# Performance work log

Hardware: AMD Instinct MI355X
Metric: run time of the kernel (lower is better)

## Reference

```python
import jax, jax.numpy as jnp
import numpy as np

N_NODES = 100000
N_EDGES = 1600000
IN_F = 128
OUT_F = 64
DROP_P = 0.1


def setup_inputs() -> dict:
    key = jax.random.key(0)
    ks = jax.random.split(key, 7)
    x = jax.random.normal(ks[0], (N_NODES, IN_F), dtype=jnp.float32)
    row_idx = jax.random.randint(ks[1], (N_EDGES,), 0, N_NODES)
    col_idx = jax.random.randint(ks[2], (N_EDGES,), 0, N_NODES)
    # normalized-adjacency-like edge weights
    adj_vals = jax.random.uniform(ks[3], (N_EDGES,), dtype=jnp.float32)
    # deterministic dropout mask (True = keep), p = DROP_P
    drop_mask = jax.random.uniform(ks[4], (N_NODES, OUT_F)) >= DROP_P
    # nn.Linear params (PyTorch default-ish init scale)
    bound = 1.0 / np.sqrt(IN_F)
    weight = jax.random.uniform(ks[5], (IN_F, OUT_F), minval=-bound, maxval=bound, dtype=jnp.float32)
    bias = jax.random.uniform(ks[6], (OUT_F,), minval=-bound, maxval=bound, dtype=jnp.float32)
    return {"x": x, "row_idx": row_idx, "col_idx": col_idx, "adj_vals": adj_vals,
            "drop_mask": drop_mask, "weight": weight, "bias": bias}


def reference(x, row_idx, col_idx, adj_vals, drop_mask, weight, bias):
    # hidden = Linear(x)
    hidden = x @ weight + bias                      # [N, OUT_F]
    # F.dropout (training): mask + rescale by 1/(1-p)
    hidden = jnp.where(drop_mask, hidden * (1.0 / (1.0 - DROP_P)), 0.0)
    # spmm(adj, hidden): gather source rows, scale by edge weight, scatter-add to dest rows
    msgs = adj_vals[:, None] * hidden[col_idx]      # [E, OUT_F]
    support = jax.ops.segment_sum(msgs, row_idx, num_segments=N_NODES)  # [N, OUT_F]
    # act(support); adj is passed through unchanged in the original, so return activated features
    return jax.nn.relu(support)
```

## Files before the change

### kernel.cpp

```cpp
#include <hip/hip_runtime.h>
#include <hip/hip_bf16.h>

#define N_NODES 100000
#define IN_F    128
#define OUT_F   64
#define INV_KEEP (1.0f / 0.9f)

#define RPB_LOG 7
#define RPB (1 << RPB_LOG)
#define NB  ((N_NODES + RPB - 1) / RPB)
#define CAP 3072
#define BIN_CHUNK 4096
#define BIN_BS 1024
#define ACC_BS 1024
#define ACC_CHUNK 2560

typedef __attribute__((ext_vector_type(8))) short bf16x8;
typedef __attribute__((ext_vector_type(4))) float f32x4;

__device__ __forceinline__ unsigned bf16rne(float f) {
  unsigned u = __float_as_uint(f);
  u += 0x7FFFu + ((u >> 16) & 1u);
  return u >> 16;
}

__global__ __launch_bounds__(256) void wtrans_kernel(
    const float* __restrict__ w, ushort* __restrict__ wt) {
  __shared__ float wsl[IN_F][OUT_F + 1];
  const int t = threadIdx.x;
  #pragma unroll
  for (int i = 0; i < 8; ++i) {
    const int fi = t + i * 256;
    const float4 v = ((const float4*)w)[fi];
    const int fl = 4 * fi;
    const int k = fl >> 6;
    const int c = fl & 63;
    wsl[k][c] = v.x; wsl[k][c + 1] = v.y; wsl[k][c + 2] = v.z; wsl[k][c + 3] = v.w;
  }
  __syncthreads();
  const int c = t >> 2;
  const int k0 = (t & 3) * 32;
  unsigned hw[16];
  #pragma unroll
  for (int i = 0; i < 16; ++i) {
    const unsigned u0 = bf16rne(wsl[k0 + 2 * i][c]);
    const unsigned u1 = bf16rne(wsl[k0 + 2 * i + 1][c]);
    hw[i] = u0 | (u1 << 16);
  }
  uint4* dst = (uint4*)(wt + (size_t)c * IN_F + k0);
  dst[0] = make_uint4(hw[0], hw[1], hw[2], hw[3]);
  dst[1] = make_uint4(hw[4], hw[5], hw[6], hw[7]);
  dst[2] = make_uint4(hw[8], hw[9], hw[10], hw[11]);
  dst[3] = make_uint4(hw[12], hw[13], hw[14], hw[15]);
}

__global__ __launch_bounds__(256) void gemm_dropout_kernel(
    const float* __restrict__ x, const ushort* __restrict__ wt,
    const float* __restrict__ bias, const void* __restrict__ mask,
    ushort* __restrict__ hidden, int* __restrict__ cursor) {
  __shared__ float tileT[64][68];
  __shared__ int mask_is_u8;

  const int tid = threadIdx.x;
  const int wv = tid >> 6;
  const int l = tid & 63;
  const int rowbase = blockIdx.x * 64;

  if (blockIdx.x == 0 && tid < 196) {
    const int c0 = 4 * tid;
    ((int4*)cursor)[tid] =
        make_int4(c0 * CAP, (c0 + 1) * CAP, (c0 + 2) * CAP, (c0 + 3) * CAP);
  }

  if (tid < 64) {
    const unsigned char* m8 = (const unsigned char*)mask;
    unsigned long long b = __ballot(m8[tid] != 0);
    if (tid == 0) mask_is_u8 = (__popcll(b) > 32) ? 1 : 0;
  }

  const int col = l & 15;
  const int kg = l >> 4;

  int arow = rowbase + 16 * wv + col;
  if (arow >= N_NODES) arow = N_NODES - 1;
  const float* xrow = x + (size_t)arow * IN_F;

  float4 xa[4], xb[4];
  #pragma unroll
  for (int s = 0; s < 4; ++s) {
    xa[s] = *(const float4*)(xrow + 32 * s + 8 * kg);
    xb[s] = *(const float4*)(xrow + 32 * s + 8 * kg + 4);
  }

  bf16x8 bfr[4][4];
  #pragma unroll
  for (int c = 0; c < 4; ++c)
    #pragma unroll
    for (int s = 0; s < 4; ++s)
      bfr[c][s] =
          *(const bf16x8*)(wt + (size_t)(16 * c + col) * IN_F + 32 * s + 8 * kg);

  f32x4 acc0 = {0.f, 0.f, 0.f, 0.f};
  f32x4 acc1 = {0.f, 0.f, 0.f, 0.f};
  f32x4 acc2 = {0.f, 0.f, 0.f, 0.f};
  f32x4 acc3 = {0.f, 0.f, 0.f, 0.f};

  #pragma unroll
  for (int s = 0; s < 4; ++s) {
    const float f[8] = {xa[s].x, xa[s].y, xa[s].z, xa[s].w,
                        xb[s].x, xb[s].y, xb[s].z, xb[s].w};
    bf16x8 ahi, alo;
    #pragma unroll
    for (int j = 0; j < 8; ++j) {
      const unsigned h = bf16rne(f[j]);
      ahi[j] = (short)h;
      const float lo = f[j] - __uint_as_float(h << 16);
      alo[j] = (short)bf16rne(lo);
    }
    acc0 = __builtin_amdgcn_mfma_f32_16x16x32_bf16(ahi, bfr[0][s], acc0, 0, 0, 0);
    acc1 = __builtin_amdgcn_mfma_f32_16x16x32_bf16(ahi, bfr[1][s], acc1, 0, 0, 0);
    acc2 = __builtin_amdgcn_mfma_f32_16x16x32_bf16(ahi, bfr[2][s], acc2, 0, 0, 0);
    acc3 = __builtin_amdgcn_mfma_f32_16x16x32_bf16(ahi, bfr[3][s], acc3, 0, 0, 0);
    acc0 = __builtin_amdgcn_mfma_f32_16x16x32_bf16(alo, bfr[0][s], acc0, 0, 0, 0);
    acc1 = __builtin_amdgcn_mfma_f32_16x16x32_bf16(alo, bfr[1][s], acc1, 0, 0, 0);
    acc2 = __builtin_amdgcn_mfma_f32_16x16x32_bf16(alo, bfr[2][s], acc2, 0, 0, 0);
    acc3 = __builtin_amdgcn_mfma_f32_16x16x32_bf16(alo, bfr[3][s], acc3, 0, 0, 0);
  }

  #pragma unroll
  for (int r = 0; r < 4; ++r) {
    const int lr = 16 * wv + 4 * kg + r;
    tileT[lr][0 + col]  = acc0[r];
    tileT[lr][16 + col] = acc1[r];
    tileT[lr][32 + col] = acc2[r];
    tileT[lr][48 + col] = acc3[r];
  }
  __syncthreads();

  const unsigned char* m8 = (const unsigned char*)mask;
  const int* m32 = (const int*)mask;
  const int u8mode = mask_is_u8;

  #pragma unroll
  for (int i = 0; i < 2; ++i) {
    const int item = tid + i * 256;
    const int r2 = item >> 3;
    const int cq = (item & 7) * 8;
    const int grow = rowbase + r2;
    if (grow < N_NODES) {
      const float4 b0 = *(const float4*)&bias[cq];
      const float4 b1 = *(const float4*)&bias[cq + 4];
      const float4 v0 = *(const float4*)&tileT[r2][cq];
      const float4 v1 = *(const float4*)&tileT[r2][cq + 4];
      const float vals[8] = {v0.x + b0.x, v0.y + b0.y, v0.z + b0.z, v0.w + b0.w,
                             v1.x + b1.x, v1.y + b1.y, v1.z + b1.z, v1.w + b1.w};
      unsigned keep[8];
      const size_t mbase = (size_t)grow * OUT_F + cq;
      if (u8mode) {
        const uint2 mv = *(const uint2*)(m8 + mbase);
        #pragma unroll
        for (int b = 0; b < 4; ++b) {
          keep[0 + b] = (mv.x >> (8 * b)) & 255u;
          keep[4 + b] = (mv.y >> (8 * b)) & 255u;
        }
      } else {
        const int4 mv0 = *(const int4*)(m32 + mbase);
        const int4 mv1 = *(const int4*)(m32 + mbase + 4);
        keep[0] = (unsigned)mv0.x; keep[1] = (unsigned)mv0.y;
        keep[2] = (unsigned)mv0.z; keep[3] = (unsigned)mv0.w;
        keep[4] = (unsigned)mv1.x; keep[5] = (unsigned)mv1.y;
        keep[6] = (unsigned)mv1.z; keep[7] = (unsigned)mv1.w;
      }
      unsigned hw[4];
      #pragma unroll
      for (int p = 0; p < 4; ++p) {
        const float w0 = keep[2 * p]     ? vals[2 * p] * INV_KEEP     : 0.f;
        const float w1 = keep[2 * p + 1] ? vals[2 * p + 1] * INV_KEEP : 0.f;
        hw[p] = bf16rne(w0) | (bf16rne(w1) << 16);
      }
      *(uint4*)&hidden[mbase] = make_uint4(hw[0], hw[1], hw[2], hw[3]);
    }
  }
}

__global__ __launch_bounds__(BIN_BS) void bin_kernel(
    const int* __restrict__ row_idx, const int* __restrict__ col_idx,
    const float* __restrict__ adj, int* __restrict__ cursor,
    int2* __restrict__ packed, int nedges) {
  __shared__ unsigned sMeta[BIN_CHUNK];
  __shared__ float    sAdj[BIN_CHUNK];
  __shared__ ushort   sBkt[BIN_CHUNK];
  __shared__ int      sCnt[1024];
  __shared__ int      sScan[1024];
  __shared__ int      sBase[1024];
  __shared__ int      sFill[1024];

  const int t = threadIdx.x;
  const int e0 = blockIdx.x * BIN_CHUNK;
  const int n = min(BIN_CHUNK, nedges - e0);

  sCnt[t] = 0;
  sBase[t] = 0;
  sFill[t] = 0;
  __syncthreads();

  int      eb[4];
  unsigned em[4];
  float    ea[4];
  #pragma unroll
  for (int j = 0; j < 4; ++j) {
    const int idx = t + j * BIN_BS;
    eb[j] = -1;
    if (idx < n) {
      const int r = row_idx[e0 + idx];
      const int c = col_idx[e0 + idx];
      ea[j] = adj[e0 + idx];
      eb[j] = r >> RPB_LOG;
      em[j] = ((unsigned)(r & (RPB - 1)) << 17) | (unsigned)c;
      atomicAdd(&sCnt[eb[j]], 1);
    }
  }
  __syncthreads();

  const int v = sCnt[t];
  sScan[t] = v;
  __syncthreads();
  int a = v;
  #pragma unroll
  for (int d = 1; d < 1024; d <<= 1) {
    const int add = (t >= d) ? sScan[t - d] : 0;
    __syncthreads();
    a += add;
    sScan[t] = a;
    __syncthreads();
  }
  const int excl = a - v;
  sScan[t] = excl;
  if (v > 0 && t < NB) sBase[t] = atomicAdd(&cursor[t], v);
  __syncthreads();

  #pragma unroll
  for (int j = 0; j < 4; ++j) {
    if (eb[j] >= 0) {
      const int p = sScan[eb[j]] + atomicAdd(&sFill[eb[j]], 1);
      sMeta[p] = em[j];
      sAdj[p] = ea[j];
      sBkt[p] = (ushort)eb[j];
    }
  }
  __syncthreads();

  #pragma unroll
  for (int j = 0; j < 4; ++j) {
    const int sp = t + j * BIN_BS;
    if (sp < n) {
      const int b = sBkt[sp];
      const int dst = sBase[b] + (sp - sScan[b]);
      int2 o;
      o.x = (int)sMeta[sp];
      o.y = __float_as_int(sAdj[sp]);
      packed[dst] = o;
    }
  }
}

__global__ __launch_bounds__(ACC_BS) void bucket_acc_kernel(
    const int* __restrict__ cursor, const int2* __restrict__ packed,
    const ushort* __restrict__ hidden, float* __restrict__ out) {
  __shared__ float accT[RPB * OUT_F];
  __shared__ int2  sEdge[ACC_CHUNK];
  __shared__ int   rowCnt[RPB];
  __shared__ int   rowOff[RPB + 1];
  __shared__ int   sTmp[RPB];

  const int t = threadIdx.x;
  const int b = blockIdx.x;
  const int lane = t & 63;
  const int h  = lane >> 5;
  const int q  = (lane >> 4) & 1;
  const int fl = lane & 15;
  const int wv = t >> 6;

  const uint2* __restrict__ hid64 = (const uint2*)hidden;

  float4* a4 = (float4*)accT;
  #pragma unroll
  for (int i = 0; i < 2; ++i)
    a4[t + i * ACC_BS] = make_float4(0.f, 0.f, 0.f, 0.f);

  const int s = b * CAP;
  const int e = cursor[b];

  for (int g0 = s; g0 < e; g0 += ACC_CHUNK) {
    const int n = min(ACC_CHUNK, e - g0);

    if (t < RPB) rowCnt[t] = 0;
    __syncthreads();

    int2 ev[3];
    int  ro[3], pos[3];
    #pragma unroll
    for (int j = 0; j < 3; ++j) {
      const int idx = t + j * ACC_BS;
      ro[j] = -1;
      if (idx < n) {
        ev[j] = packed[g0 + idx];
        ro[j] = (int)(((unsigned)ev[j].x >> 17) & (RPB - 1));
        pos[j] = atomicAdd(&rowCnt[ro[j]], 1);
      }
    }
    __syncthreads();

    if (t < RPB) sTmp[t] = rowCnt[t];
    __syncthreads();
    for (int d = 1; d < RPB; d <<= 1) {
      int add = 0;
      if (t < RPB && t >= d) add = sTmp[t - d];
      __syncthreads();
      if (t < RPB) sTmp[t] += add;
      __syncthreads();
    }
    if (t < RPB) rowOff[t] = sTmp[t] - rowCnt[t];
    if (t == 0) rowOff[RPB] = n;
    __syncthreads();

    #pragma unroll
    for (int j = 0; j < 3; ++j) {
      if (ro[j] >= 0) sEdge[rowOff[ro[j]] + pos[j]] = ev[j];
    }
    __syncthreads();

    for (int pr = 0; pr < 4; ++pr) {
      const int r = wv * 8 + 2 * pr + h;
      const int rs = rowOff[r];
      const int re = rowOff[r + 1];
      float acc0 = 0.f, acc1 = 0.f, acc2 = 0.f, acc3 = 0.f;
      int i = rs + q;
      while (__any(i < re)) {
        const bool v0 = i < re;
        const bool v1 = i + 2 < re;
        const int2 e0 = sEdge[v0 ? i : 0];
        const int2 e1 = sEdge[v1 ? i + 2 : 0];
        const uint2 g0v = hid64[((unsigned)e0.x & 0x1FFFFu) * 16 + fl];
        const uint2 g1v = hid64[((unsigned)e1.x & 0x1FFFFu) * 16 + fl];
        const float a0 = v0 ? __int_as_float(e0.y) : 0.f;
        const float a1 = v1 ? __int_as_float(e1.y) : 0.f;
        acc0 = fmaf(a0, __uint_as_float(g0v.x << 16), acc0);
        acc1 = fmaf(a0, __uint_as_float(g0v.x & 0xFFFF0000u), acc1);
        acc2 = fmaf(a0, __uint_as_float(g0v.y << 16), acc2);
        acc3 = fmaf(a0, __uint_as_float(g0v.y & 0xFFFF0000u), acc3);
        acc0 = fmaf(a1, __uint_as_float(g1v.x << 16), acc0);
        acc1 = fmaf(a1, __uint_as_float(g1v.x & 0xFFFF0000u), acc1);
        acc2 = fmaf(a1, __uint_as_float(g1v.y << 16), acc2);
        acc3 = fmaf(a1, __uint_as_float(g1v.y & 0xFFFF0000u), acc3);
        i += 4;
      }
      acc0 += __shfl_xor(acc0, 16);
      acc1 += __shfl_xor(acc1, 16);
      acc2 += __shfl_xor(acc2, 16);
      acc3 += __shfl_xor(acc3, 16);
      if (q == 0) {
        float4* dst = (float4*)&accT[r * OUT_F + 4 * fl];
        float4 v = *dst;
        v.x += acc0; v.y += acc1; v.z += acc2; v.w += acc3;
        *dst = v;
      }
    }
    __syncthreads();
  }

  __syncthreads();
  const int rbase = b * RPB;
  float4* o4 = (float4*)(out + (size_t)rbase * OUT_F);
  #pragma unroll
  for (int i = 0; i < 2; ++i) {
    const int idx4 = t + i * ACC_BS;
    const int r = idx4 >> 4;
    if (rbase + r < N_NODES) {
      float4 vv = a4[idx4];
      vv.x = fmaxf(vv.x, 0.f);
      vv.y = fmaxf(vv.y, 0.f);
      vv.z = fmaxf(vv.z, 0.f);
      vv.w = fmaxf(vv.w, 0.f);
      o4[idx4] = vv;
    }
  }
}

extern "C" void kernel_launch(void* const* d_in, const int* in_sizes, int n_in,
                              void* d_out, int out_size, void* d_ws,
                              size_t ws_size, hipStream_t stream) {
  const float* x       = (const float*)d_in[0];
  const int*   row_idx = (const int*)d_in[1];
  const int*   col_idx = (const int*)d_in[2];
  const float* adj     = (const float*)d_in[3];
  const void*  mask    = d_in[4];
  const float* w       = (const float*)d_in[5];
  const float* bias    = (const float*)d_in[6];
  float* out = (float*)d_out;
  const int nedges = in_sizes[1];

  char* ws = (char*)d_ws;
  const size_t off_hidden = 0;
  const size_t sz_hidden  = (size_t)N_NODES * OUT_F * sizeof(ushort);
  const size_t off_cursor = (off_hidden + sz_hidden + 15) & ~(size_t)15;
  const size_t off_packed = (off_cursor + 784 * 4 + 15) & ~(size_t)15;
  const size_t sz_packed  = (size_t)NB * CAP * 8;
  const size_t off_wt     = (off_packed + sz_packed + 15) & ~(size_t)15;

  ushort* hidden = (ushort*)(ws + off_hidden);
  int*    cursor = (int*)(ws + off_cursor);
  int2*   packed = (int2*)(ws + off_packed);
  ushort* wt     = (ushort*)(ws + off_wt);

  wtrans_kernel<<<1, 256, 0, stream>>>(w, wt);
  gemm_dropout_kernel<<<(N_NODES + 63) / 64, 256, 0, stream>>>(
      x, wt, bias, mask, hidden, cursor);
  bin_kernel<<<(nedges + BIN_CHUNK - 1) / BIN_CHUNK, BIN_BS, 0, stream>>>(
      row_idx, col_idx, adj, cursor, packed, nedges);
  bucket_acc_kernel<<<NB, ACC_BS, 0, stream>>>(cursor, packed, hidden, out);
}
```

Baseline: 87.63 us.

## Fuse edge binning into GEMM-dropout kernel and move cursor init

Merges the edge bucketing pass into the GEMM/dropout kernel. Each 256-thread block first produces its 64 hidden rows, then bins 1024 edges, reusing the same shared memory. The 1024-wide block scan is replaced by a wavefront shuffle scan over four buckets per thread, and cursor initialisation moves into the weight-transpose kernel. This removes one kernel launch and lets binning overlap with GEMM work across blocks. In exchange it adds a barrier to the GEMM blocks, uses smaller edge chunks that issue more global cursor atomics, and hard-codes a grid size that must cover both nodes and edges.

```diff
diff --git a/kernel.cpp b/kernel.cpp
--- a/kernel.cpp
+++ b/kernel.cpp
@@ -9,11 +9,12 @@
 #define RPB_LOG 7
 #define RPB (1 << RPB_LOG)
 #define NB  ((N_NODES + RPB - 1) / RPB)
+#define NBP 784
 #define CAP 3072
-#define BIN_CHUNK 4096
-#define BIN_BS 1024
+#define EPB 1024
 #define ACC_BS 1024
 #define ACC_CHUNK 2560
+#define NGRID 1563
 
 typedef __attribute__((ext_vector_type(8))) short bf16x8;
 typedef __attribute__((ext_vector_type(4))) float f32x4;
@@ -25,9 +26,17 @@
 }
 
 __global__ __launch_bounds__(256) void wtrans_kernel(
-    const float* __restrict__ w, ushort* __restrict__ wt) {
+    const float* __restrict__ w, ushort* __restrict__ wt,
+    int* __restrict__ cursor) {
   __shared__ float wsl[IN_F][OUT_F + 1];
   const int t = threadIdx.x;
+
+  if (t < 196) {
+    const int c0 = 4 * t;
+    ((int4*)cursor)[t] =
+        make_int4(c0 * CAP, (c0 + 1) * CAP, (c0 + 2) * CAP, (c0 + 3) * CAP);
+  }
+
   #pragma unroll
   for (int i = 0; i < 8; ++i) {
     const int fi = t + i * 256;
@@ -54,11 +63,13 @@
   dst[3] = make_uint4(hw[12], hw[13], hw[14], hw[15]);
 }
 
-__global__ __launch_bounds__(256) void gemm_dropout_kernel(
+__global__ __launch_bounds__(256) void gemm_bin_kernel(
     const float* __restrict__ x, const ushort* __restrict__ wt,
     const float* __restrict__ bias, const void* __restrict__ mask,
-    ushort* __restrict__ hidden, int* __restrict__ cursor) {
-  __shared__ float tileT[64][68];
+    ushort* __restrict__ hidden, const int* __restrict__ row_idx,
+    const int* __restrict__ col_idx, const float* __restrict__ adj,
+    int* __restrict__ cursor, int2* __restrict__ packed, int nedges) {
+  __shared__ __align__(16) char smem[22848];
   __shared__ int mask_is_u8;
 
   const int tid = threadIdx.x;
@@ -66,11 +77,7 @@
   const int l = tid & 63;
   const int rowbase = blockIdx.x * 64;
 
-  if (blockIdx.x == 0 && tid < 196) {
-    const int c0 = 4 * tid;
-    ((int4*)cursor)[tid] =
-        make_int4(c0 * CAP, (c0 + 1) * CAP, (c0 + 2) * CAP, (c0 + 3) * CAP);
-  }
+  float (*tileT)[68] = (float(*)[68])smem;
 
   if (tid < 64) {
     const unsigned char* m8 = (const unsigned char*)mask;
@@ -137,129 +144,147 @@
   }
   __syncthreads();
 
-  const unsigned char* m8 = (const unsigned char*)mask;
-  const int* m32 = (const int*)mask;
-  const int u8mode = mask_is_u8;
-
-  #pragma unroll
-  for (int i = 0; i < 2; ++i) {
-    const int item = tid + i * 256;
-    const int r2 = item >> 3;
-    const int cq = (item & 7) * 8;
-    const int grow = rowbase + r2;
-    if (grow < N_NODES) {
-      const float4 b0 = *(const float4*)&bias[cq];
-      const float4 b1 = *(const float4*)&bias[cq + 4];
-      const float4 v0 = *(const float4*)&tileT[r2][cq];
-      const float4 v1 = *(const float4*)&tileT[r2][cq + 4];
-      const float vals[8] = {v0.x + b0.x, v0.y + b0.y, v0.z + b0.z, v0.w + b0.w,
-                             v1.x + b1.x, v1.y + b1.y, v1.z + b1.z, v1.w + b1.w};
-      unsigned keep[8];
-      const size_t mbase = (size_t)grow * OUT_F + cq;
-      if (u8mode) {
-        const uint2 mv = *(const uint2*)(m8 + mbase);
+  {
+    const unsigned char* m8 = (const unsigned char*)mask;
+    const int* m32 = (const int*)mask;
+    const int u8mode = mask_is_u8;
+
+    #pragma unroll
+    for (int i = 0; i < 2; ++i) {
+      const int item = tid + i * 256;
+      const int r2 = item >> 3;
+      const int cq = (item & 7) * 8;
+      const int grow = rowbase + r2;
+      if (grow < N_NODES) {
+        const float4 b0 = *(const float4*)&bias[cq];
+        const float4 b1 = *(const float4*)&bias[cq + 4];
+        const float4 v0 = *(const float4*)&tileT[r2][cq];
+        const float4 v1 = *(const float4*)&tileT[r2][cq + 4];
+        const float vals[8] = {v0.x + b0.x, v0.y + b0.y, v0.z + b0.z,
+                               v0.w + b0.w, v1.x + b1.x, v1.y + b1.y,
+                               v1.z + b1.z, v1.w + b1.w};
+        unsigned keep[8];
+        const size_t mbase = (size_t)grow * OUT_F + cq;
+        if (u8mode) {
+          const uint2 mv = *(const uint2*)(m8 + mbase);
+          #pragma unroll
+          for (int b = 0; b < 4; ++b) {
+            keep[0 + b] = (mv.x >> (8 * b)) & 255u;
+            keep[4 + b] = (mv.y >> (8 * b)) & 255u;
+          }
+        } else {
+          const int4 mv0 = *(const int4*)(m32 + mbase);
+          const int4 mv1 = *(const int4*)(m32 + mbase + 4);
+          keep[0] = (unsigned)mv0.x; keep[1] = (unsigned)mv0.y;
+          keep[2] = (unsigned)mv0.z; keep[3] = (unsigned)mv0.w;
+          keep[4] = (unsigned)mv1.x; keep[5] = (unsigned)mv1.y;
+          keep[6] = (unsigned)mv1.z; keep[7] = (unsigned)mv1.w;
+        }
+        unsigned hw[4];
         #pragma unroll
-        for (int b = 0; b < 4; ++b) {
-          keep[0 + b] = (mv.x >> (8 * b)) & 255u;
-          keep[4 + b] = (mv.y >> (8 * b)) & 255u;
+        for (int p = 0; p < 4; ++p) {
+          const float w0 = keep[2 * p]     ? vals[2 * p] * INV_KEEP     : 0.f;
+          const float w1 = keep[2 * p + 1] ? vals[2 * p + 1] * INV_KEEP : 0.f;
+          hw[p] = bf16rne(w0) | (bf16rne(w1) << 16);
         }
-      } else {
-        const int4 mv0 = *(const int4*)(m32 + mbase);
-        const int4 mv1 = *(const int4*)(m32 + mbase + 4);
-        keep[0] = (unsigned)mv0.x; keep[1] = (unsigned)mv0.y;
-        keep[2] = (unsigned)mv0.z; keep[3] = (unsigned)mv0.w;
-        keep[4] = (unsigned)mv1.x; keep[5] = (unsigned)mv1.y;
-        keep[6] = (unsigned)mv1.z; keep[7] = (unsigned)mv1.w;
-      }
-      unsigned hw[4];
+        *(uint4*)&hidden[mbase] = make_uint4(hw[0], hw[1], hw[2], hw[3]);
+      }
+    }
+  }
+  __syncthreads();
+
+  const int e0 = blockIdx.x * EPB;
+  if (e0 < nedges) {
+    unsigned* sMeta = (unsigned*)(smem);
+    float*    sAdj  = (float*)(smem + 4096);
+    ushort*   sBkt  = (ushort*)(smem + 8192);
+    int*      sCnt  = (int*)(smem + 10240);
+    int*      sScan = (int*)(smem + 13376);
+    int*      sBase = (int*)(smem + 16512);
+    int*      sFill = (int*)(smem + 19648);
+    int*      sWS   = (int*)(smem + 22784);
+
+    const int n = min(EPB, nedges - e0);
+
+    for (int i = tid; i < NBP; i += 256) { sCnt[i] = 0; sFill[i] = 0; }
+    __syncthreads();
+
+    int      eb[4];
+    unsigned em[4];
+    float    ea[4];
+    #pragma unroll
+    for (int j = 0; j < 4; ++j) {
+      const int idx = tid + j * 256;
+      eb[j] = -1;
+      if (idx < n) {
+        const int r = row_idx[e0 + idx];
+        const int c = col_idx[e0 + idx];
+        ea[j] = adj[e0 + idx];
+        eb[j] = r >> RPB_LOG;
+        em[j] = ((unsigned)(r & (RPB - 1)) << 17) | (unsigned)c;
+        atomicAdd(&sCnt[eb[j]], 1);
+      }
+    }
+    __syncthreads();
+
+    {
+      int c0 = 0, c1 = 0, c2 = 0, c3 = 0;
+      if (tid < 196) {
+        c0 = sCnt[4 * tid];
+        c1 = sCnt[4 * tid + 1];
+        c2 = sCnt[4 * tid + 2];
+        c3 = sCnt[4 * tid + 3];
+      }
+      const int T = c0 + c1 + c2 + c3;
+      int sc = T;
       #pragma unroll
-      for (int p = 0; p < 4; ++p) {
-        const float w0 = keep[2 * p]     ? vals[2 * p] * INV_KEEP     : 0.f;
-        const float w1 = keep[2 * p + 1] ? vals[2 * p + 1] * INV_KEEP : 0.f;
-        hw[p] = bf16rne(w0) | (bf16rne(w1) << 16);
-      }
-      *(uint4*)&hidden[mbase] = make_uint4(hw[0], hw[1], hw[2], hw[3]);
-    }
-  }
-}
-
-__global__ __launch_bounds__(BIN_BS) void bin_kernel(
-    const int* __restrict__ row_idx, const int* __restrict__ col_idx,
-    const float* __restrict__ adj, int* __restrict__ cursor,
-    int2* __restrict__ packed, int nedges) {
-  __shared__ unsigned sMeta[BIN_CHUNK];
-  __shared__ float    sAdj[BIN_CHUNK];
-  __shared__ ushort   sBkt[BIN_CHUNK];
-  __shared__ int      sCnt[1024];
-  __shared__ int      sScan[1024];
-  __shared__ int      sBase[1024];
-  __shared__ int      sFill[1024];
-
-  const int t = threadIdx.x;
-  const int e0 = blockIdx.x * BIN_CHUNK;
-  const int n = min(BIN_CHUNK, nedges - e0);
-
-  sCnt[t] = 0;
-  sBase[t] = 0;
-  sFill[t] = 0;
-  __syncthreads();
-
-  int      eb[4];
-  unsigned em[4];
-  float    ea[4];
-  #pragma unroll
-  for (int j = 0; j < 4; ++j) {
-    const int idx = t + j * BIN_BS;
-    eb[j] = -1;
-    if (idx < n) {
-      const int r = row_idx[e0 + idx];
-      const int c = col_idx[e0 + idx];
-      ea[j] = adj[e0 + idx];
-      eb[j] = r >> RPB_LOG;
-      em[j] = ((unsigned)(r & (RPB - 1)) << 17) | (unsigned)c;
-      atomicAdd(&sCnt[eb[j]], 1);
-    }
-  }
-  __syncthreads();
-
-  const int v = sCnt[t];
-  sScan[t] = v;
-  __syncthreads();
-  int a = v;
-  #pragma unroll
-  for (int d = 1; d < 1024; d <<= 1) {
-    const int add = (t >= d) ? sScan[t - d] : 0;
-    __syncthreads();
-    a += add;
-    sScan[t] = a;
-    __syncthreads();
-  }
-  const int excl = a - v;
-  sScan[t] = excl;
-  if (v > 0 && t < NB) sBase[t] = atomicAdd(&cursor[t], v);
-  __syncthreads();
-
-  #pragma unroll
-  for (int j = 0; j < 4; ++j) {
-    if (eb[j] >= 0) {
-      const int p = sScan[eb[j]] + atomicAdd(&sFill[eb[j]], 1);
-      sMeta[p] = em[j];
-      sAdj[p] = ea[j];
-      sBkt[p] = (ushort)eb[j];
-    }
-  }
-  __syncthreads();
-
-  #pragma unroll
-  for (int j = 0; j < 4; ++j) {
-    const int sp = t + j * BIN_BS;
-    if (sp < n) {
-      const int b = sBkt[sp];
-      const int dst = sBase[b] + (sp - sScan[b]);
-      int2 o;
-      o.x = (int)sMeta[sp];
-      o.y = __float_as_int(sAdj[sp]);
-      packed[dst] = o;
+      for (int d = 1; d < 64; d <<= 1) {
+        const int u = __shfl_up(sc, d);
+        if (l >= d) sc += u;
+      }
+      if (l == 63) sWS[wv] = sc;
+      __syncthreads();
+      if (tid == 0) {
+        const int w0 = sWS[0], w1 = sWS[1], w2 = sWS[2];
+        sWS[4] = 0; sWS[5] = w0; sWS[6] = w0 + w1; sWS[7] = w0 + w1 + w2;
+      }
+      __syncthreads();
+      if (tid < 196) {
+        const int ex = sc - T + sWS[4 + wv];
+        const int b0 = 4 * tid;
+        sScan[b0]     = ex;
+        sScan[b0 + 1] = ex + c0;
+        sScan[b0 + 2] = ex + c0 + c1;
+        sScan[b0 + 3] = ex + c0 + c1 + c2;
+        if (c0 > 0 && b0 < NB)     sBase[b0]     = atomicAdd(&cursor[b0], c0);
+        if (c1 > 0 && b0 + 1 < NB) sBase[b0 + 1] = atomicAdd(&cursor[b0 + 1], c1);
+        if (c2 > 0 && b0 + 2 < NB) sBase[b0 + 2] = atomicAdd(&cursor[b0 + 2], c2);
+        if (c3 > 0 && b0 + 3 < NB) sBase[b0 + 3] = atomicAdd(&cursor[b0 + 3], c3);
+      }
+    }
+    __syncthreads();
+
+    #pragma unroll
+    for (int j = 0; j < 4; ++j) {
+      if (eb[j] >= 0) {
+        const int p = sScan[eb[j]] + atomicAdd(&sFill[eb[j]], 1);
+        sMeta[p] = em[j];
+        sAdj[p] = ea[j];
+        sBkt[p] = (ushort)eb[j];
+      }
+    }
+    __syncthreads();
+
+    #pragma unroll
+    for (int j = 0; j < 4; ++j) {
+      const int sp = tid + j * 256;
+      if (sp < n) {
+        const int b = sBkt[sp];
+        int2 o;
+        o.x = (int)sMeta[sp];
+        o.y = __float_as_int(sAdj[sp]);
+        packed[sBase[b] + (sp - sScan[b])] = o;
+      }
     }
   }
 }
@@ -404,7 +429,7 @@
   const size_t off_hidden = 0;
   const size_t sz_hidden  = (size_t)N_NODES * OUT_F * sizeof(ushort);
   const size_t off_cursor = (off_hidden + sz_hidden + 15) & ~(size_t)15;
-  const size_t off_packed = (off_cursor + 784 * 4 + 15) & ~(size_t)15;
+  const size_t off_packed = (off_cursor + NBP * 4 + 15) & ~(size_t)15;
   const size_t sz_packed  = (size_t)NB * CAP * 8;
   const size_t off_wt     = (off_packed + sz_packed + 15) & ~(size_t)15;
 
@@ -413,10 +438,8 @@
   int2*   packed = (int2*)(ws + off_packed);
   ushort* wt     = (ushort*)(ws + off_wt);
 
-  wtrans_kernel<<<1, 256, 0, stream>>>(w, wt);
-  gemm_dropout_kernel<<<(N_NODES + 63) / 64, 256, 0, stream>>>(
-      x, wt, bias, mask, hidden, cursor);
-  bin_kernel<<<(nedges + BIN_CHUNK - 1) / BIN_CHUNK, BIN_BS, 0, stream>>>(
-      row_idx, col_idx, adj, cursor, packed, nedges);
+  wtrans_kernel<<<1, 256, 0, stream>>>(w, wt, cursor);
+  gemm_bin_kernel<<<NGRID, 256, 0, stream>>>(
+      x, wt, bias, mask, hidden, row_idx, col_idx, adj, cursor, packed, nedges);
   bucket_acc_kernel<<<NB, ACC_BS, 0, stream>>>(cursor, packed, hidden, out);
 }
```

Result: slower. 182.6 us (+108.4%).
